# Performance work log

Hardware: AMD Instinct MI355X
Metric: run time of the kernel (lower is better)

## Reference

```python
import jax, jax.numpy as jnp
import numpy as np

IN_F = 4096
OUT_F = 4096
B, T = 4, 2048
KQ = 16  # 16*16*16 == IN_F
SCALE = 1.0


def setup_inputs() -> dict:
    key = jax.random.key(0)
    ks = jax.random.split(key, 8)
    x = jax.random.normal(ks[0], (B, T, IN_F), jnp.float32)
    # SVD factors of a frozen weight W [out,in]: U [out,r], S [r], V [r,in], r=min(in,out)
    U = jax.random.normal(ks[1], (OUT_F, IN_F), jnp.float32) / np.sqrt(IN_F).astype(np.float32)
    S = jax.random.uniform(ks[2], (IN_F,), jnp.float32)
    V = jax.random.normal(ks[3], (IN_F, IN_F), jnp.float32) / np.sqrt(IN_F).astype(np.float32)
    # delta initialized to 1e-3 in the torch module
    delta = jnp.full((OUT_F,), 1e-3, jnp.float32)
    # kron_Q factors initialized near identity (torch init is exact identity)
    kron_Q1 = jnp.eye(KQ, dtype=jnp.float32) + 0.01 * jax.random.normal(ks[4], (KQ, KQ), jnp.float32)
    kron_Q2 = jnp.eye(KQ, dtype=jnp.float32) + 0.01 * jax.random.normal(ks[5], (KQ, KQ), jnp.float32)
    kron_Q3 = jnp.eye(KQ, dtype=jnp.float32) + 0.01 * jax.random.normal(ks[6], (KQ, KQ), jnp.float32)
    return {"x": x, "U": U, "S": S, "V": V, "delta": delta,
            "kron_Q1": kron_Q1, "kron_Q2": kron_Q2, "kron_Q3": kron_Q3}


def reference(x, U, S, V, delta, kron_Q1, kron_Q2, kron_Q3):
    # S' = relu(S + delta); W = U @ diag(S') @ V  (diag fused as column scale of U)
    S_eff = jax.nn.relu(S + delta)
    W = (U * S_eff[None, :]) @ V                      # [out, in]
    # orthogonal_matrix = kron(kron(Q1, Q2), Q3)     # [in, in]
    ortho = jnp.kron(jnp.kron(kron_Q1, kron_Q2), kron_Q3)
    W_t = ortho @ W.T                                 # [in, out]
    # F.linear(x, W_t.t()) == x @ W_t ; dropout is identity in eval mode
    out = x @ W_t                                     # [B, T, out]
    return out * SCALE
```

## Files before the change

kernel.cpp:

```cpp
#include <hip/hip_runtime.h>
#include <stdint.h>
#include <stddef.h>

typedef short v8s __attribute__((ext_vector_type(8)));
typedef float v4f __attribute__((ext_vector_type(4)));
typedef unsigned short v4u16 __attribute__((ext_vector_type(4)));

__device__ __forceinline__ unsigned short f2bf(float f) {
  union { float f; uint32_t u; } v; v.f = f;
  uint32_t r = (v.u + 0x7FFFu + ((v.u >> 16) & 1u)) >> 16;
  return (unsigned short)r;
}

__device__ __forceinline__ void gl_lds16(const void* g, void* l) {
  __builtin_amdgcn_global_load_lds(
      (__attribute__((address_space(1))) void*)(uintptr_t)(g),
      (__attribute__((address_space(3))) void*)(uintptr_t)(l), 16, 0, 0);
}

__global__ __launch_bounds__(256) void k_prep_us(const float* __restrict__ U,
                                                 const float* __restrict__ S,
                                                 const float* __restrict__ delta,
                                                 unsigned short* __restrict__ Us) {
  int idx = blockIdx.x * 256 + threadIdx.x;
  int e0 = idx * 8;
  int col = e0 & 4095;
  float4 u0 = *(const float4*)(U + e0);
  float4 u1 = *(const float4*)(U + e0 + 4);
  float4 s0 = *(const float4*)(S + col);
  float4 s1 = *(const float4*)(S + col + 4);
  float4 d0 = *(const float4*)(delta + col);
  float4 d1 = *(const float4*)(delta + col + 4);
  float uu[8] = {u0.x, u0.y, u0.z, u0.w, u1.x, u1.y, u1.z, u1.w};
  float se[8] = {s0.x + d0.x, s0.y + d0.y, s0.z + d0.z, s0.w + d0.w,
                 s1.x + d1.x, s1.y + d1.y, s1.z + d1.z, s1.w + d1.w};
  v8s o;
#pragma unroll
  for (int j = 0; j < 8; ++j) {
    float sv = se[j] > 0.f ? se[j] : 0.f;
    o[j] = (short)f2bf(uu[j] * sv);
  }
  *(v8s*)(Us + e0) = o;
}

__global__ __launch_bounds__(256) void k_prep_x(const float* __restrict__ in,
                                                unsigned short* __restrict__ out) {
  int idx = blockIdx.x * 256 + threadIdx.x;
  int e0 = idx * 8;
  float4 a = *(const float4*)(in + e0);
  float4 b = *(const float4*)(in + e0 + 4);
  float f[8] = {a.x, a.y, a.z, a.w, b.x, b.y, b.z, b.w};
  v8s o;
#pragma unroll
  for (int j = 0; j < 8; ++j) o[j] = (short)f2bf(f[j]);
  *(v8s*)(out + e0) = o;
}

__device__ __forceinline__ int PADI(int e) { return e + 4 * (e >> 6); }

__global__ __launch_bounds__(256) void k_kron(const float* __restrict__ V,
                                              const float* __restrict__ Q1,
                                              const float* __restrict__ Q2,
                                              const float* __restrict__ Q3,
                                              unsigned short* __restrict__ Vo) {
  __shared__ float bufA[4352];
  __shared__ float bufB[4352];
  __shared__ float q1s[256], q2s[256], q3s[256];
  int t = threadIdx.x;
  int row = blockIdx.x;
  q1s[t] = Q1[t]; q2s[t] = Q2[t]; q3s[t] = Q3[t];
  const float* vrow = V + (size_t)row * 4096;
#pragma unroll
  for (int i = 0; i < 4; ++i) {
    int idx = t + i * 256;
    float4 v = ((const float4*)vrow)[idx];
    int e = idx * 4;
    *(float4*)&bufA[PADI(e)] = v;
  }
  __syncthreads();
  {
    float r[16];
    int base = PADI(t * 16);
#pragma unroll
    for (int j3 = 0; j3 < 16; ++j3) r[j3] = bufA[base + j3];
#pragma unroll
    for (int i3 = 0; i3 < 16; ++i3) {
      float s = 0.f;
#pragma unroll
      for (int j3 = 0; j3 < 16; ++j3) s += r[j3] * q3s[i3 * 16 + j3];
      bufB[base + i3] = s;
    }
  }
  __syncthreads();
  {
    int j1 = t >> 4, i3 = t & 15;
    float r[16];
#pragma unroll
    for (int j2 = 0; j2 < 16; ++j2) r[j2] = bufB[PADI(j1 * 256 + j2 * 16 + i3)];
#pragma unroll
    for (int i2 = 0; i2 < 16; ++i2) {
      float s = 0.f;
#pragma unroll
      for (int j2 = 0; j2 < 16; ++j2) s += r[j2] * q2s[i2 * 16 + j2];
      bufA[PADI(j1 * 256 + i2 * 16 + i3)] = s;
    }
  }
  __syncthreads();
  {
    int i2 = t >> 4, i3 = t & 15;
    float r[16];
#pragma unroll
    for (int j1 = 0; j1 < 16; ++j1) r[j1] = bufA[PADI(j1 * 256 + i2 * 16 + i3)];
    unsigned short* orow = Vo + (size_t)row * 4096;
#pragma unroll
    for (int i1 = 0; i1 < 16; ++i1) {
      float s = 0.f;
#pragma unroll
      for (int j1 = 0; j1 < 16; ++j1) s += r[j1] * q1s[i1 * 16 + j1];
      orow[i1 * 256 + i2 * 16 + i3] = f2bf(s);
    }
  }
}

__global__ __launch_bounds__(256) void k_transpose(const unsigned short* __restrict__ in,
                                                   unsigned short* __restrict__ out) {
  __shared__ unsigned short tile[64][68];
  int bx = blockIdx.x & 63;
  int by = blockIdx.x >> 6;
  int t = threadIdx.x;
#pragma unroll
  for (int q = 0; q < 4; ++q) {
    int i = t + q * 256;
    int r = i >> 4;
    int c = (i & 15) * 4;
    v4u16 v = *(const v4u16*)(in + (size_t)(by * 64 + r) * 4096 + bx * 64 + c);
    tile[r][c] = v[0]; tile[r][c + 1] = v[1]; tile[r][c + 2] = v[2]; tile[r][c + 3] = v[3];
  }
  __syncthreads();
#pragma unroll
  for (int q = 0; q < 4; ++q) {
    int i = t + q * 256;
    int r = i >> 4;
    int c = (i & 15) * 4;
    v4u16 v;
    v[0] = tile[c][r]; v[1] = tile[c + 1][r]; v[2] = tile[c + 2][r]; v[3] = tile[c + 3][r];
    *(v4u16*)(out + (size_t)(bx * 64 + r) * 4096 + by * 64 + c) = v;
  }
}


#define STG(P0, P1, REGI, TT, KH) do {                                   \
    const unsigned short* _s0 = (P0) + (TT) * 64 + (KH) * 32;            \
    const unsigned short* _s1 = (P1) + (TT) * 64 + (KH) * 32;            \
    gl_lds16(_s0, &lds[(REGI) * 8192 + tid * 8]);                        \
    gl_lds16(_s1, &lds[(REGI) * 8192 + 4096 + tid * 8]);                 \
  } while (0)

#define RDA(BUF, KK, H, I) \
  (*(const v8s*)&lds[((BUF) * 2 + (KK)) * 8192 + (wr * 128 + (H) * 64 + (I) * 16) * 32 + acb])
#define RDB(BUF, KK, NN) \
  (*(const v8s*)&lds[(4 + (BUF) * 2 + (KK)) * 8192 + (wc * 64 + (NN) * 16) * 32 + acb])

#define MM(I, NN, AV, BV) \
  acc[(I)][(NN)] = __builtin_amdgcn_mfma_f32_16x16x32_bf16(AV, BV, acc[(I)][(NN)], 0, 0, 0)

#define PH(BUF, KK, H, STAGES, DOVM) do {                                 \
    v8s a0 = RDA(BUF, KK, H, 0), a1 = RDA(BUF, KK, H, 1);                 \
    v8s a2 = RDA(BUF, KK, H, 2), a3 = RDA(BUF, KK, H, 3);                 \
    if ((H) == 0) {                                                       \
      b0 = RDB(BUF, KK, 0); b1 = RDB(BUF, KK, 1);                         \
      b2 = RDB(BUF, KK, 2); b3 = RDB(BUF, KK, 3);                         \
    }                                                                     \
    STAGES;                                                               \
    __builtin_amdgcn_s_barrier();                                         \
    __builtin_amdgcn_s_setprio(1);                                        \
    MM((H)*4+0, 0, a0, b0); MM((H)*4+1, 0, a1, b0);                       \
    MM((H)*4+2, 0, a2, b0); MM((H)*4+3, 0, a3, b0);                       \
    MM((H)*4+0, 1, a0, b1); MM((H)*4+1, 1, a1, b1);                       \
    MM((H)*4+2, 1, a2, b1); MM((H)*4+3, 1, a3, b1);                       \
    MM((H)*4+0, 2, a0, b2); MM((H)*4+1, 2, a1, b2);                       \
    MM((H)*4+2, 2, a2, b2); MM((H)*4+3, 2, a3, b2);                       \
    MM((H)*4+0, 3, a0, b3); MM((H)*4+1, 3, a1, b3);                       \
    MM((H)*4+2, 3, a2, b3); MM((H)*4+3, 3, a3, b3);                       \
    __builtin_amdgcn_s_setprio(0);                                        \
    if (DOVM) asm volatile("s_waitcnt vmcnt(6)" ::: "memory");            \
    __builtin_amdgcn_s_barrier();                                         \
  } while (0)

template <int OUT_BF16>
__global__ __launch_bounds__(512, 2) void k_gemm256(const unsigned short* __restrict__ A,
                                                    const unsigned short* __restrict__ B,
                                                    void* __restrict__ Cv,
                                                    int K, int N, int nbn) {
  __shared__ unsigned short lds[65536];
  const int NT = K >> 6;
  int nwg = gridDim.x;
  int bid = blockIdx.x;
  int wg = (bid & 7) * (nwg >> 3) + (bid >> 3);
  int bm = wg / nbn, bn = wg % nbn;
  int tid = threadIdx.x;
  int lane = tid & 63;
  int wid = tid >> 6;
  int wr = wid >> 2, wc = wid & 3;

  const unsigned short* Ab = A + (size_t)bm * 256 * K;
  const unsigned short* Bb = B + (size_t)bn * 256 * K;

  int srow = tid >> 2;
  int scol = 8 * ((tid & 3) ^ ((tid >> 3) & 3));
  const unsigned short* As0 = Ab + (size_t)srow * K + scol;
  const unsigned short* As1 = As0 + (size_t)128 * K;
  const unsigned short* Bs0 = Bb + (size_t)srow * K + scol;
  const unsigned short* Bs1 = Bs0 + (size_t)128 * K;

  int acb = (lane & 15) * 32 + (((((lane >> 4) << 4) ^ ((((lane & 15) >> 1) & 3) << 4)) >> 1));

  v4f acc[8][4];
#pragma unroll
  for (int i = 0; i < 8; ++i)
#pragma unroll
    for (int j = 0; j < 4; ++j) acc[i][j] = (v4f){0.f, 0.f, 0.f, 0.f};
  v8s b0 = {}, b1 = {}, b2 = {}, b3 = {};

  STG(Bs0, Bs1, 4, 0, 0); STG(As0, As1, 0, 0, 0);
  STG(Bs0, Bs1, 5, 0, 1); STG(As0, As1, 1, 0, 1);
  STG(Bs0, Bs1, 6, 1, 0); STG(As0, As1, 2, 1, 0);
  STG(Bs0, Bs1, 7, 1, 1);
  asm volatile("s_waitcnt vmcnt(6)" ::: "memory");
  __builtin_amdgcn_s_barrier();

  for (int it = 0; it < NT / 2; ++it) {
    int t1 = 2 * it + 1;
    int s0 = (2 * it + 2) & (NT - 1);
    int s1 = (2 * it + 3) & (NT - 1);
    PH(0, 0, 0, STG(As0, As1, 3, t1, 1), 0);
    PH(0, 0, 1, STG(Bs0, Bs1, 4, s0, 0), 0);
    PH(0, 1, 0, STG(As0, As1, 0, s0, 0), 0);
    PH(0, 1, 1, STG(Bs0, Bs1, 5, s0, 1), 1);
    PH(1, 0, 0, STG(As0, As1, 1, s0, 1), 0);
    PH(1, 0, 1, STG(Bs0, Bs1, 6, s1, 0), 0);
    PH(1, 1, 0, STG(As0, As1, 2, s1, 0), 0);
    PH(1, 1, 1, STG(Bs0, Bs1, 7, s1, 1), 1);
  }
  asm volatile("s_waitcnt vmcnt(0)" ::: "memory");

  int row0 = bm * 256 + wr * 128 + ((lane >> 4) << 2);
  int col0 = bn * 256 + wc * 64 + (lane & 15);
  if (OUT_BF16) {
    unsigned short* Cp = (unsigned short*)Cv;
#pragma unroll
    for (int m = 0; m < 8; ++m)
#pragma unroll
      for (int n = 0; n < 4; ++n)
#pragma unroll
        for (int r = 0; r < 4; ++r)
          Cp[(size_t)(row0 + m * 16 + r) * N + col0 + n * 16] = f2bf(acc[m][n][r]);
  } else {
    float* Cp = (float*)Cv;
#pragma unroll
    for (int m = 0; m < 8; ++m)
#pragma unroll
      for (int n = 0; n < 4; ++n)
#pragma unroll
        for (int r = 0; r < 4; ++r)
          Cp[(size_t)(row0 + m * 16 + r) * N + col0 + n * 16] = acc[m][n][r];
  }
}

extern "C" void kernel_launch(void* const* d_in, const int* in_sizes, int n_in,
                              void* d_out, int out_size, void* d_ws, size_t ws_size,
                              hipStream_t stream) {
  const float* x = (const float*)d_in[0];
  const float* U = (const float*)d_in[1];
  const float* S = (const float*)d_in[2];
  const float* V = (const float*)d_in[3];
  const float* delta = (const float*)d_in[4];
  const float* Q1 = (const float*)d_in[5];
  const float* Q2 = (const float*)d_in[6];
  const float* Q3 = (const float*)d_in[7];

  char* ws = (char*)d_ws;
  unsigned short* Us = (unsigned short*)(ws);
  unsigned short* Mt = (unsigned short*)(ws + 33554432);
  unsigned short* xb = (unsigned short*)(ws + 67108864);
  char* oc = (char*)d_out;
  unsigned short* Vo = (unsigned short*)(oc);
  unsigned short* VoT = (unsigned short*)(oc + 33554432);
  float* out = (float*)d_out;

  k_prep_us<<<8192, 256, 0, stream>>>(U, S, delta, Us);
  k_kron<<<4096, 256, 0, stream>>>(V, Q1, Q2, Q3, Vo);
  k_transpose<<<4096, 256, 0, stream>>>(Vo, VoT);
  k_prep_x<<<16384, 256, 0, stream>>>(x, xb);
  k_gemm256<1><<<256, 512, 0, stream>>>(Us, VoT, (void*)Mt, 4096, 4096, 16);
  k_gemm256<0><<<512, 512, 0, stream>>>(xb, Mt, (void*)out, 4096, 4096, 16);
}
```

Baseline: 470.9 us.

## Double-buffer LDS fragment registers to prefetch next phase during MFMAs

Restructures the GEMM main loop so the A/B fragments for the next phase are read from LDS into a second register set while the current phase's MFMAs run, instead of reading them before the barrier. The vmcnt wait moves ahead of the barrier so the prefetch reads see completed global-to-LDS loads. This aims to hide LDS read latency behind matrix math, at the cost of extra VGPRs (two fragment sets) and a more delicate ordering between buffer reuse and the async stage loads.

```diff
diff --git a/kernel.cpp b/kernel.cpp
--- a/kernel.cpp
+++ b/kernel.cpp
@@ -161,29 +161,33 @@
 #define RDB(BUF, KK, NN) \
   (*(const v8s*)&lds[(4 + (BUF) * 2 + (KK)) * 8192 + (wc * 64 + (NN) * 16) * 32 + acb])
 
+#define LDA_SET(S, BUF, KK, H) do {                                       \
+    aF[S][0] = RDA(BUF, KK, H, 0); aF[S][1] = RDA(BUF, KK, H, 1);         \
+    aF[S][2] = RDA(BUF, KK, H, 2); aF[S][3] = RDA(BUF, KK, H, 3);         \
+  } while (0)
+#define LDB_SET(S, BUF, KK) do {                                          \
+    bF[S][0] = RDB(BUF, KK, 0); bF[S][1] = RDB(BUF, KK, 1);               \
+    bF[S][2] = RDB(BUF, KK, 2); bF[S][3] = RDB(BUF, KK, 3);               \
+  } while (0)
+
 #define MM(I, NN, AV, BV) \
   acc[(I)][(NN)] = __builtin_amdgcn_mfma_f32_16x16x32_bf16(AV, BV, acc[(I)][(NN)], 0, 0, 0)
 
-#define PH(BUF, KK, H, STAGES, DOVM) do {                                 \
-    v8s a0 = RDA(BUF, KK, H, 0), a1 = RDA(BUF, KK, H, 1);                 \
-    v8s a2 = RDA(BUF, KK, H, 2), a3 = RDA(BUF, KK, H, 3);                 \
-    if ((H) == 0) {                                                       \
-      b0 = RDB(BUF, KK, 0); b1 = RDB(BUF, KK, 1);                         \
-      b2 = RDB(BUF, KK, 2); b3 = RDB(BUF, KK, 3);                         \
-    }                                                                     \
+#define PHASE(H, AS, BS, PRE, STAGES, DOVM) do {                          \
     STAGES;                                                               \
+    if (DOVM) asm volatile("s_waitcnt vmcnt(6)" ::: "memory");            \
     __builtin_amdgcn_s_barrier();                                         \
+    PRE;                                                                  \
     __builtin_amdgcn_s_setprio(1);                                        \
-    MM((H)*4+0, 0, a0, b0); MM((H)*4+1, 0, a1, b0);                       \
-    MM((H)*4+2, 0, a2, b0); MM((H)*4+3, 0, a3, b0);                       \
-    MM((H)*4+0, 1, a0, b1); MM((H)*4+1, 1, a1, b1);                       \
-    MM((H)*4+2, 1, a2, b1); MM((H)*4+3, 1, a3, b1);                       \
-    MM((H)*4+0, 2, a0, b2); MM((H)*4+1, 2, a1, b2);                       \
-    MM((H)*4+2, 2, a2, b2); MM((H)*4+3, 2, a3, b2);                       \
-    MM((H)*4+0, 3, a0, b3); MM((H)*4+1, 3, a1, b3);                       \
-    MM((H)*4+2, 3, a2, b3); MM((H)*4+3, 3, a3, b3);                       \
+    MM((H)*4+0, 0, aF[AS][0], bF[BS][0]); MM((H)*4+1, 0, aF[AS][1], bF[BS][0]); \
+    MM((H)*4+2, 0, aF[AS][2], bF[BS][0]); MM((H)*4+3, 0, aF[AS][3], bF[BS][0]); \
+    MM((H)*4+0, 1, aF[AS][0], bF[BS][1]); MM((H)*4+1, 1, aF[AS][1], bF[BS][1]); \
+    MM((H)*4+2, 1, aF[AS][2], bF[BS][1]); MM((H)*4+3, 1, aF[AS][3], bF[BS][1]); \
+    MM((H)*4+0, 2, aF[AS][0], bF[BS][2]); MM((H)*4+1, 2, aF[AS][1], bF[BS][2]); \
+    MM((H)*4+2, 2, aF[AS][2], bF[BS][2]); MM((H)*4+3, 2, aF[AS][3], bF[BS][2]); \
+    MM((H)*4+0, 3, aF[AS][0], bF[BS][3]); MM((H)*4+1, 3, aF[AS][1], bF[BS][3]); \
+    MM((H)*4+2, 3, aF[AS][2], bF[BS][3]); MM((H)*4+3, 3, aF[AS][3], bF[BS][3]); \
     __builtin_amdgcn_s_setprio(0);                                        \
-    if (DOVM) asm volatile("s_waitcnt vmcnt(6)" ::: "memory");            \
     __builtin_amdgcn_s_barrier();                                         \
   } while (0)
 
@@ -220,7 +224,8 @@
   for (int i = 0; i < 8; ++i)
 #pragma unroll
     for (int j = 0; j < 4; ++j) acc[i][j] = (v4f){0.f, 0.f, 0.f, 0.f};
-  v8s b0 = {}, b1 = {}, b2 = {}, b3 = {};
+  v8s aF[2][4];
+  v8s bF[2][4];
 
   STG(Bs0, Bs1, 4, 0, 0); STG(As0, As1, 0, 0, 0);
   STG(Bs0, Bs1, 5, 0, 1); STG(As0, As1, 1, 0, 1);
@@ -228,19 +233,21 @@
   STG(Bs0, Bs1, 7, 1, 1);
   asm volatile("s_waitcnt vmcnt(6)" ::: "memory");
   __builtin_amdgcn_s_barrier();
+  LDA_SET(0, 0, 0, 0);
+  LDB_SET(0, 0, 0);
 
   for (int it = 0; it < NT / 2; ++it) {
     int t1 = 2 * it + 1;
     int s0 = (2 * it + 2) & (NT - 1);
     int s1 = (2 * it + 3) & (NT - 1);
-    PH(0, 0, 0, STG(As0, As1, 3, t1, 1), 0);
-    PH(0, 0, 1, STG(Bs0, Bs1, 4, s0, 0), 0);
-    PH(0, 1, 0, STG(As0, As1, 0, s0, 0), 0);
-    PH(0, 1, 1, STG(Bs0, Bs1, 5, s0, 1), 1);
-    PH(1, 0, 0, STG(As0, As1, 1, s0, 1), 0);
-    PH(1, 0, 1, STG(Bs0, Bs1, 6, s1, 0), 0);
-    PH(1, 1, 0, STG(As0, As1, 2, s1, 0), 0);
-    PH(1, 1, 1, STG(Bs0, Bs1, 7, s1, 1), 1);
+    PHASE(0, 0, 0, LDA_SET(1, 0, 0, 1),                    STG(As0, As1, 3, t1, 1), 0);
+    PHASE(1, 1, 0, LDA_SET(0, 0, 1, 0); LDB_SET(1, 0, 1),  STG(Bs0, Bs1, 4, s0, 0), 0);
+    PHASE(0, 0, 1, LDA_SET(1, 0, 1, 1),                    STG(As0, As1, 0, s0, 0), 0);
+    PHASE(1, 1, 1, LDA_SET(0, 1, 0, 0); LDB_SET(0, 1, 0),  STG(Bs0, Bs1, 5, s0, 1), 1);
+    PHASE(0, 0, 0, LDA_SET(1, 1, 0, 1),                    STG(As0, As1, 1, s0, 1), 0);
+    PHASE(1, 1, 0, LDA_SET(0, 1, 1, 0); LDB_SET(1, 1, 1),  STG(Bs0, Bs1, 6, s1, 0), 0);
+    PHASE(0, 0, 1, LDA_SET(1, 1, 1, 1),                    STG(As0, As1, 2, s1, 0), 0);
+    PHASE(1, 1, 1, LDA_SET(0, 0, 0, 0); LDB_SET(0, 0, 0),  STG(Bs0, Bs1, 7, s1, 1), 1);
   }
   asm volatile("s_waitcnt vmcnt(0)" ::: "memory");
 
```

Result: no change. 466.3 us (-1.0%).

## Load B operand directly from global into registers, bypassing LDS

Applied to the files above, without the earlier changes.

The GEMM kernel now stages only the A tile through LDS. Each wave loads its B fragments straight from global memory into a 4-slot register ring using inline global_load_dwordx4, and the pipeline schedule and vmcnt waits are reworked to match. This halves LDS usage and removes the LDS write/read traffic for B. In exchange it adds many vector registers, issues uncoalesced per-wave B loads that repeat across the two wave rows, and depends on hand-tuned vmcnt counts being correct alongside asm loads the compiler cannot track.

```diff
diff --git a/kernel.cpp b/kernel.cpp
--- a/kernel.cpp
+++ b/kernel.cpp
@@ -149,42 +149,44 @@
 }
 
 
-#define STG(P0, P1, REGI, TT, KH) do {                                   \
-    const unsigned short* _s0 = (P0) + (TT) * 64 + (KH) * 32;            \
-    const unsigned short* _s1 = (P1) + (TT) * 64 + (KH) * 32;            \
-    gl_lds16(_s0, &lds[(REGI) * 8192 + tid * 8]);                        \
-    gl_lds16(_s1, &lds[(REGI) * 8192 + 4096 + tid * 8]);                 \
+#define STGA(RI, TT, KK) do {                                             \
+    const unsigned short* _s0 = As0 + (TT) * 64 + (KK) * 32;              \
+    const unsigned short* _s1 = As1 + (TT) * 64 + (KK) * 32;              \
+    gl_lds16(_s0, &lds[(RI) * 8192 + tid * 8]);                           \
+    gl_lds16(_s1, &lds[(RI) * 8192 + 4096 + tid * 8]);                    \
   } while (0)
 
-#define RDA(BUF, KK, H, I) \
-  (*(const v8s*)&lds[((BUF) * 2 + (KK)) * 8192 + (wr * 128 + (H) * 64 + (I) * 16) * 32 + acb])
-#define RDB(BUF, KK, NN) \
-  (*(const v8s*)&lds[(4 + (BUF) * 2 + (KK)) * 8192 + (wc * 64 + (NN) * 16) * 32 + acb])
+#define BLOAD(SL, TT, KK) do {                                            \
+    int _o = (TT) * 64 + (KK) * 32;                                       \
+    asm volatile("global_load_dwordx4 %0, %1, off" : "=v"(bG[SL][0]) : "v"(Bb0 + _o)); \
+    asm volatile("global_load_dwordx4 %0, %1, off" : "=v"(bG[SL][1]) : "v"(Bb1 + _o)); \
+    asm volatile("global_load_dwordx4 %0, %1, off" : "=v"(bG[SL][2]) : "v"(Bb2 + _o)); \
+    asm volatile("global_load_dwordx4 %0, %1, off" : "=v"(bG[SL][3]) : "v"(Bb3 + _o)); \
+  } while (0)
+
+#define RDA2(RI, H, I) \
+  (*(const v8s*)&lds[(RI) * 8192 + (wr * 128 + (H) * 64 + (I) * 16) * 32 + acb])
 
 #define MM(I, NN, AV, BV) \
   acc[(I)][(NN)] = __builtin_amdgcn_mfma_f32_16x16x32_bf16(AV, BV, acc[(I)][(NN)], 0, 0, 0)
 
-#define PH(BUF, KK, H, STAGES, DOVM) do {                                 \
-    v8s a0 = RDA(BUF, KK, H, 0), a1 = RDA(BUF, KK, H, 1);                 \
-    v8s a2 = RDA(BUF, KK, H, 2), a3 = RDA(BUF, KK, H, 3);                 \
-    if ((H) == 0) {                                                       \
-      b0 = RDB(BUF, KK, 0); b1 = RDB(BUF, KK, 1);                         \
-      b2 = RDB(BUF, KK, 2); b3 = RDB(BUF, KK, 3);                         \
-    }                                                                     \
-    STAGES;                                                               \
+#define PHX(RI, H, SL, ISSUES, DOVM) do {                                 \
+    v8s _a0 = RDA2(RI, H, 0), _a1 = RDA2(RI, H, 1);                       \
+    v8s _a2 = RDA2(RI, H, 2), _a3 = RDA2(RI, H, 3);                       \
+    ISSUES;                                                               \
+    __builtin_amdgcn_s_setprio(1);                                        \
+    MM((H)*4+0, 0, _a0, bG[SL][0]); MM((H)*4+1, 0, _a1, bG[SL][0]);       \
+    MM((H)*4+2, 0, _a2, bG[SL][0]); MM((H)*4+3, 0, _a3, bG[SL][0]);       \
+    MM((H)*4+0, 1, _a0, bG[SL][1]); MM((H)*4+1, 1, _a1, bG[SL][1]);       \
+    MM((H)*4+2, 1, _a2, bG[SL][1]); MM((H)*4+3, 1, _a3, bG[SL][1]);       \
+    MM((H)*4+0, 2, _a0, bG[SL][2]); MM((H)*4+1, 2, _a1, bG[SL][2]);       \
+    MM((H)*4+2, 2, _a2, bG[SL][2]); MM((H)*4+3, 2, _a3, bG[SL][2]);       \
+    MM((H)*4+0, 3, _a0, bG[SL][3]); MM((H)*4+1, 3, _a1, bG[SL][3]);       \
+    MM((H)*4+2, 3, _a2, bG[SL][3]); MM((H)*4+3, 3, _a3, bG[SL][3]);       \
+    __builtin_amdgcn_s_setprio(0);                                        \
+    if (DOVM) asm volatile("s_waitcnt vmcnt(12)" ::: "memory");           \
     __builtin_amdgcn_s_barrier();                                         \
-    __builtin_amdgcn_s_setprio(1);                                        \
-    MM((H)*4+0, 0, a0, b0); MM((H)*4+1, 0, a1, b0);                       \
-    MM((H)*4+2, 0, a2, b0); MM((H)*4+3, 0, a3, b0);                       \
-    MM((H)*4+0, 1, a0, b1); MM((H)*4+1, 1, a1, b1);                       \
-    MM((H)*4+2, 1, a2, b1); MM((H)*4+3, 1, a3, b1);                       \
-    MM((H)*4+0, 2, a0, b2); MM((H)*4+1, 2, a1, b2);                       \
-    MM((H)*4+2, 2, a2, b2); MM((H)*4+3, 2, a3, b2);                       \
-    MM((H)*4+0, 3, a0, b3); MM((H)*4+1, 3, a1, b3);                       \
-    MM((H)*4+2, 3, a2, b3); MM((H)*4+3, 3, a3, b3);                       \
-    __builtin_amdgcn_s_setprio(0);                                        \
-    if (DOVM) asm volatile("s_waitcnt vmcnt(6)" ::: "memory");            \
-    __builtin_amdgcn_s_barrier();                                         \
+    __builtin_amdgcn_sched_barrier(0);                                    \
   } while (0)
 
 template <int OUT_BF16>
@@ -192,8 +194,9 @@
                                                     const unsigned short* __restrict__ B,
                                                     void* __restrict__ Cv,
                                                     int K, int N, int nbn) {
-  __shared__ unsigned short lds[65536];
+  __shared__ unsigned short lds[32768];
   const int NT = K >> 6;
+  const int NM = NT - 1;
   int nwg = gridDim.x;
   int bid = blockIdx.x;
   int wg = (bid & 7) * (nwg >> 3) + (bid >> 3);
@@ -210,8 +213,11 @@
   int scol = 8 * ((tid & 3) ^ ((tid >> 3) & 3));
   const unsigned short* As0 = Ab + (size_t)srow * K + scol;
   const unsigned short* As1 = As0 + (size_t)128 * K;
-  const unsigned short* Bs0 = Bb + (size_t)srow * K + scol;
-  const unsigned short* Bs1 = Bs0 + (size_t)128 * K;
+
+  const unsigned short* Bb0 = Bb + (size_t)(wc * 64 + (lane & 15)) * K + (lane >> 4) * 8;
+  const unsigned short* Bb1 = Bb0 + (size_t)16 * K;
+  const unsigned short* Bb2 = Bb0 + (size_t)32 * K;
+  const unsigned short* Bb3 = Bb0 + (size_t)48 * K;
 
   int acb = (lane & 15) * 32 + (((((lane >> 4) << 4) ^ ((((lane & 15) >> 1) & 3) << 4)) >> 1));
 
@@ -220,27 +226,26 @@
   for (int i = 0; i < 8; ++i)
 #pragma unroll
     for (int j = 0; j < 4; ++j) acc[i][j] = (v4f){0.f, 0.f, 0.f, 0.f};
-  v8s b0 = {}, b1 = {}, b2 = {}, b3 = {};
-
-  STG(Bs0, Bs1, 4, 0, 0); STG(As0, As1, 0, 0, 0);
-  STG(Bs0, Bs1, 5, 0, 1); STG(As0, As1, 1, 0, 1);
-  STG(Bs0, Bs1, 6, 1, 0); STG(As0, As1, 2, 1, 0);
-  STG(Bs0, Bs1, 7, 1, 1);
-  asm volatile("s_waitcnt vmcnt(6)" ::: "memory");
+  v8s bG[4][4];
+
+  STGA(0, 0, 0); STGA(1, 0, 1); STGA(2, 1, 0);
+  BLOAD(0, 0, 0); BLOAD(1, 0, 1); BLOAD(2, 1, 0);
+  asm volatile("s_waitcnt vmcnt(8)" ::: "memory");
   __builtin_amdgcn_s_barrier();
+  __builtin_amdgcn_sched_barrier(0);
 
   for (int it = 0; it < NT / 2; ++it) {
     int t1 = 2 * it + 1;
-    int s0 = (2 * it + 2) & (NT - 1);
-    int s1 = (2 * it + 3) & (NT - 1);
-    PH(0, 0, 0, STG(As0, As1, 3, t1, 1), 0);
-    PH(0, 0, 1, STG(Bs0, Bs1, 4, s0, 0), 0);
-    PH(0, 1, 0, STG(As0, As1, 0, s0, 0), 0);
-    PH(0, 1, 1, STG(Bs0, Bs1, 5, s0, 1), 1);
-    PH(1, 0, 0, STG(As0, As1, 1, s0, 1), 0);
-    PH(1, 0, 1, STG(Bs0, Bs1, 6, s1, 0), 0);
-    PH(1, 1, 0, STG(As0, As1, 2, s1, 0), 0);
-    PH(1, 1, 1, STG(Bs0, Bs1, 7, s1, 1), 1);
+    int s0 = (2 * it + 2) & NM;
+    int s1 = (2 * it + 3) & NM;
+    PHX(0, 0, 0, { STGA(3, t1, 1); BLOAD(3, t1, 1); }, 0);
+    PHX(0, 1, 0, {}, 1);
+    PHX(1, 0, 1, { STGA(0, s0, 0); BLOAD(0, s0, 0); }, 0);
+    PHX(1, 1, 1, {}, 1);
+    PHX(2, 0, 2, { STGA(1, s0, 1); BLOAD(1, s0, 1); }, 0);
+    PHX(2, 1, 2, {}, 1);
+    PHX(3, 0, 3, { STGA(2, s1, 0); BLOAD(2, s1, 0); }, 0);
+    PHX(3, 1, 3, {}, 1);
   }
   asm volatile("s_waitcnt vmcnt(0)" ::: "memory");
 
```

Measured after the change: 633.0 us. 34.4% more time.

## Switch GEMM inner loop to 32x32x16 bf16 MFMA with reworked LDS staging schedule

Applied to the files above, without the earlier changes.

Replaces the 16x16x32 MFMA tiles with 32x32x16 MFMA, so each wave holds a 4x2 grid of 32x32 accumulators instead of 8x4 of 16x16. LDS reads become fewer and wider per phase, using a new XOR-swizzled addressing scheme. The global-to-LDS staging order and vmcnt wait counts are rearranged so two k-halves are consumed per register slot. The aim is fewer LDS reads and MFMA issue overhead per FLOP. The cost is a more intricate staging schedule that could introduce races or bank conflicts, and the output store pattern changes.

```diff
diff --git a/kernel.cpp b/kernel.cpp
--- a/kernel.cpp
+++ b/kernel.cpp
@@ -4,6 +4,7 @@
 
 typedef short v8s __attribute__((ext_vector_type(8)));
 typedef float v4f __attribute__((ext_vector_type(4)));
+typedef float v16f __attribute__((ext_vector_type(16)));
 typedef unsigned short v4u16 __attribute__((ext_vector_type(4)));
 
 __device__ __forceinline__ unsigned short f2bf(float f) {
@@ -156,34 +157,25 @@
     gl_lds16(_s1, &lds[(REGI) * 8192 + 4096 + tid * 8]);                 \
   } while (0)
 
-#define RDA(BUF, KK, H, I) \
-  (*(const v8s*)&lds[((BUF) * 2 + (KK)) * 8192 + (wr * 128 + (H) * 64 + (I) * 16) * 32 + acb])
-#define RDB(BUF, KK, NN) \
-  (*(const v8s*)&lds[(4 + (BUF) * 2 + (KK)) * 8192 + (wc * 64 + (NN) * 16) * 32 + acb])
-
-#define MM(I, NN, AV, BV) \
-  acc[(I)][(NN)] = __builtin_amdgcn_mfma_f32_16x16x32_bf16(AV, BV, acc[(I)][(NN)], 0, 0, 0)
-
-#define PH(BUF, KK, H, STAGES, DOVM) do {                                 \
-    v8s a0 = RDA(BUF, KK, H, 0), a1 = RDA(BUF, KK, H, 1);                 \
-    v8s a2 = RDA(BUF, KK, H, 2), a3 = RDA(BUF, KK, H, 3);                 \
-    if ((H) == 0) {                                                       \
-      b0 = RDB(BUF, KK, 0); b1 = RDB(BUF, KK, 1);                         \
-      b2 = RDB(BUF, KK, 2); b3 = RDB(BUF, KK, 3);                         \
-    }                                                                     \
+#define MM32(M, NN, AV, BV) \
+  acc[(M)][(NN)] = __builtin_amdgcn_mfma_f32_32x32x16_bf16(AV, BV, acc[(M)][(NN)], 0, 0, 0)
+
+#define PH(RI, KX, STAGES, DOVM) do {                                     \
+    v8s a0 = *(const v8s*)&lds[((RI) * 8192 + abase + 0 * 1024) ^ (KX)];  \
+    v8s a1 = *(const v8s*)&lds[((RI) * 8192 + abase + 1 * 1024) ^ (KX)];  \
+    v8s a2 = *(const v8s*)&lds[((RI) * 8192 + abase + 2 * 1024) ^ (KX)];  \
+    v8s a3 = *(const v8s*)&lds[((RI) * 8192 + abase + 3 * 1024) ^ (KX)];  \
+    v8s b0 = *(const v8s*)&lds[(((4 + (RI)) * 8192) + bbase + 0 * 1024) ^ (KX)]; \
+    v8s b1 = *(const v8s*)&lds[(((4 + (RI)) * 8192) + bbase + 1 * 1024) ^ (KX)]; \
     STAGES;                                                               \
     __builtin_amdgcn_s_barrier();                                         \
     __builtin_amdgcn_s_setprio(1);                                        \
-    MM((H)*4+0, 0, a0, b0); MM((H)*4+1, 0, a1, b0);                       \
-    MM((H)*4+2, 0, a2, b0); MM((H)*4+3, 0, a3, b0);                       \
-    MM((H)*4+0, 1, a0, b1); MM((H)*4+1, 1, a1, b1);                       \
-    MM((H)*4+2, 1, a2, b1); MM((H)*4+3, 1, a3, b1);                       \
-    MM((H)*4+0, 2, a0, b2); MM((H)*4+1, 2, a1, b2);                       \
-    MM((H)*4+2, 2, a2, b2); MM((H)*4+3, 2, a3, b2);                       \
-    MM((H)*4+0, 3, a0, b3); MM((H)*4+1, 3, a1, b3);                       \
-    MM((H)*4+2, 3, a2, b3); MM((H)*4+3, 3, a3, b3);                       \
+    MM32(0, 0, a0, b0); MM32(1, 0, a1, b0);                               \
+    MM32(2, 0, a2, b0); MM32(3, 0, a3, b0);                               \
+    MM32(0, 1, a0, b1); MM32(1, 1, a1, b1);                               \
+    MM32(2, 1, a2, b1); MM32(3, 1, a3, b1);                               \
     __builtin_amdgcn_s_setprio(0);                                        \
-    if (DOVM) asm volatile("s_waitcnt vmcnt(6)" ::: "memory");            \
+    if (DOVM) asm volatile("s_waitcnt vmcnt(8)" ::: "memory");            \
     __builtin_amdgcn_s_barrier();                                         \
   } while (0)
 
@@ -194,6 +186,7 @@
                                                     int K, int N, int nbn) {
   __shared__ unsigned short lds[65536];
   const int NT = K >> 6;
+  const int NM = NT - 1;
   int nwg = gridDim.x;
   int bid = blockIdx.x;
   int wg = (bid & 7) * (nwg >> 3) + (bid >> 3);
@@ -213,57 +206,64 @@
   const unsigned short* Bs0 = Bb + (size_t)srow * K + scol;
   const unsigned short* Bs1 = Bs0 + (size_t)128 * K;
 
-  int acb = (lane & 15) * 32 + (((((lane >> 4) << 4) ^ ((((lane & 15) >> 1) & 3) << 4)) >> 1));
-
-  v4f acc[8][4];
-#pragma unroll
-  for (int i = 0; i < 8; ++i)
-#pragma unroll
-    for (int j = 0; j < 4; ++j) acc[i][j] = (v4f){0.f, 0.f, 0.f, 0.f};
-  v8s b0 = {}, b1 = {}, b2 = {}, b3 = {};
+  int hi = lane >> 5;
+  int sz = (lane >> 1) & 3;
+  int rowo = (lane & 31) * 32;
+  int sl0 = (hi ^ sz) * 8;
+  int abase = rowo + wr * 4096 + sl0;
+  int bbase = rowo + wc * 2048 + sl0;
+
+  v16f acc[4][2];
+#pragma unroll
+  for (int i = 0; i < 4; ++i)
+#pragma unroll
+    for (int j = 0; j < 2; ++j)
+#pragma unroll
+      for (int r = 0; r < 16; ++r) acc[i][j][r] = 0.f;
 
   STG(Bs0, Bs1, 4, 0, 0); STG(As0, As1, 0, 0, 0);
   STG(Bs0, Bs1, 5, 0, 1); STG(As0, As1, 1, 0, 1);
   STG(Bs0, Bs1, 6, 1, 0); STG(As0, As1, 2, 1, 0);
-  STG(Bs0, Bs1, 7, 1, 1);
-  asm volatile("s_waitcnt vmcnt(6)" ::: "memory");
+  asm volatile("s_waitcnt vmcnt(8)" ::: "memory");
   __builtin_amdgcn_s_barrier();
 
   for (int it = 0; it < NT / 2; ++it) {
     int t1 = 2 * it + 1;
-    int s0 = (2 * it + 2) & (NT - 1);
-    int s1 = (2 * it + 3) & (NT - 1);
-    PH(0, 0, 0, STG(As0, As1, 3, t1, 1), 0);
-    PH(0, 0, 1, STG(Bs0, Bs1, 4, s0, 0), 0);
-    PH(0, 1, 0, STG(As0, As1, 0, s0, 0), 0);
-    PH(0, 1, 1, STG(Bs0, Bs1, 5, s0, 1), 1);
-    PH(1, 0, 0, STG(As0, As1, 1, s0, 1), 0);
-    PH(1, 0, 1, STG(Bs0, Bs1, 6, s1, 0), 0);
-    PH(1, 1, 0, STG(As0, As1, 2, s1, 0), 0);
-    PH(1, 1, 1, STG(Bs0, Bs1, 7, s1, 1), 1);
+    int s0 = (2 * it + 2) & NM;
+    int s1 = (2 * it + 3) & NM;
+    PH(0, 0,  { STG(As0, As1, 3, t1, 1); STG(Bs0, Bs1, 7, t1, 1); }, 0);
+    PH(0, 16, {}, 1);
+    PH(1, 0,  STG(As0, As1, 0, s0, 0), 0);
+    PH(1, 16, STG(Bs0, Bs1, 4, s0, 0), 1);
+    PH(2, 0,  STG(As0, As1, 1, s0, 1), 0);
+    PH(2, 16, STG(Bs0, Bs1, 5, s0, 1), 1);
+    PH(3, 0,  STG(As0, As1, 2, s1, 0), 0);
+    PH(3, 16, STG(Bs0, Bs1, 6, s1, 0), 1);
   }
   asm volatile("s_waitcnt vmcnt(0)" ::: "memory");
 
-  int row0 = bm * 256 + wr * 128 + ((lane >> 4) << 2);
-  int col0 = bn * 256 + wc * 64 + (lane & 15);
+  int rowC = bm * 256 + wr * 128 + 4 * hi;
+  int colC = bn * 256 + wc * 64 + (lane & 31);
   if (OUT_BF16) {
     unsigned short* Cp = (unsigned short*)Cv;
 #pragma unroll
-    for (int m = 0; m < 8; ++m)
-#pragma unroll
-      for (int n = 0; n < 4; ++n)
-#pragma unroll
-        for (int r = 0; r < 4; ++r)
-          Cp[(size_t)(row0 + m * 16 + r) * N + col0 + n * 16] = f2bf(acc[m][n][r]);
+    for (int m = 0; m < 4; ++m)
+#pragma unroll
+      for (int n = 0; n < 2; ++n)
+#pragma unroll
+        for (int r = 0; r < 16; ++r)
+          Cp[(size_t)(rowC + m * 32 + (r & 3) + 8 * (r >> 2)) * N + colC + n * 32] =
+              f2bf(acc[m][n][r]);
   } else {
     float* Cp = (float*)Cv;
 #pragma unroll
-    for (int m = 0; m < 8; ++m)
-#pragma unroll
-      for (int n = 0; n < 4; ++n)
-#pragma unroll
-        for (int r = 0; r < 4; ++r)
-          Cp[(size_t)(row0 + m * 16 + r) * N + col0 + n * 16] = acc[m][n][r];
+    for (int m = 0; m < 4; ++m)
+#pragma unroll
+      for (int n = 0; n < 2; ++n)
+#pragma unroll
+        for (int r = 0; r < 16; ++r)
+          Cp[(size_t)(rowC + m * 32 + (r & 3) + 8 * (r >> 2)) * N + colC + n * 32] =
+              acc[m][n][r];
   }
 }
 
```

New measurement: 508.8 us. +8.0%, slower.
